# Performance work log

Hardware: AMD Instinct MI355X
Metric: run time of the kernel (lower is better)

The kernel has to match this reference:

```python
import jax, jax.numpy as jnp
import numpy as np

TEMPERATURE = 8.0

def _non_neg(x):
    # exp(x) for x<0, x+1 for x>=0 (non-negative feature map)
    return jnp.where(x < 0, jnp.exp(x), x + 1.0)

def setup_inputs() -> dict:
    key = jax.random.key(0)
    kq, kk, kv, km = jax.random.split(key, 4)
    B, H, S, D = 8, 16, 4096, 64
    q = jax.random.normal(kq, (B, H, S, D), dtype=jnp.float32)
    k = jax.random.normal(kk, (B, H, S, D), dtype=jnp.float32)
    v = jax.random.normal(kv, (B, H, S, D), dtype=jnp.float32)
    token_mask = jax.random.randint(km, (B, S), 0, 2).astype(bool)
    return {"q": q, "k": k, "v": v, "token_mask": token_mask}

def reference(q, k, v, token_mask):
    B, H, S, D = q.shape
    idx = jnp.arange(S, dtype=q.dtype)
    cos_vec = jnp.cos(jnp.pi / 2.0 / S * idx)[:, None]  # [S,1], broadcasts over D
    sin_vec = jnp.sin(jnp.pi / 2.0 / S * idx)[:, None]
    qf = _non_neg(q)
    kf = _non_neg(k)
    q_cos = qf * cos_vec
    q_sin = qf * sin_vec
    k_cos = kf * cos_vec
    k_sin = kf * sin_vec
    mask = token_mask[:, None, :, None].astype(q.dtype)  # [B,1,S,1]
    q_cos = q_cos * mask
    q_sin = q_sin * mask
    # global context: [B,H,D,Dv]
    k_cos_v = jnp.einsum('bhsd,bhse->bhde', k_cos, v)
    k_sin_v = jnp.einsum('bhsd,bhse->bhde', k_sin, v)
    values = (jnp.einsum('bhsd,bhde->bhse', q_cos, k_cos_v)
              + jnp.einsum('bhsd,bhde->bhse', q_sin, k_sin_v)) / TEMPERATURE
    return values
```

## Files before the change

kernel.cpp:

```cpp
#include <hip/hip_runtime.h>
#include <math.h>

#define Bn 8
#define Hn 16
#define Sn 4096
#define Dn 64
#define BHn 128
#define CW 3.834951969714103e-4f

typedef __attribute__((ext_vector_type(8))) short short8;
typedef __attribute__((ext_vector_type(4))) float f32x4;

__device__ __forceinline__ unsigned short f2bf(float x) {
    unsigned int u = __float_as_uint(x);
    u += 0x7fffu + ((u >> 16) & 1u);
    return (unsigned short)(u >> 16);
}
__device__ __forceinline__ unsigned int pack2(float lo, float hi) {
    return (unsigned int)f2bf(lo) | ((unsigned int)f2bf(hi) << 16);
}
__device__ __forceinline__ float nneg(float x) {
    return x < 0.f ? __expf(x) : x + 1.f;
}

__global__ __launch_bounds__(256) void k_init(float4* kv4, int* flag,
                                              const unsigned char* mask_raw) {
    int i = blockIdx.x * 256 + threadIdx.x;
    kv4[i] = make_float4(0.f, 0.f, 0.f, 0.f);
    if (blockIdx.x == 0) {
        __shared__ int s_any;
        if (threadIdx.x == 0) s_any = 0;
        __syncthreads();
        int any = 0;
        int base = threadIdx.x * 16;
        #pragma unroll
        for (int j = 0; j < 16; j++) {
            int idx = base + j;
            if ((idx & 3) && mask_raw[idx]) any = 1;
        }
        if (any) s_any = 1;
        __syncthreads();
        if (threadIdx.x == 0) *flag = s_any ? 0 : 1;
    }
}

__global__ __launch_bounds__(256) void k_phase1(const float* __restrict__ kk,
                                                const float* __restrict__ vv,
                                                float* __restrict__ kv) {
    __shared__ unsigned int ldsKc[64 * 36];
    __shared__ unsigned int ldsKs[64 * 36];
    __shared__ unsigned int ldsV [64 * 36];
    const int t    = threadIdx.x;
    const int bh   = blockIdx.x >> 3;
    const int sblk = (blockIdx.x & 7) << 9;
    const int c    = t & 15;
    const int rp   = t >> 4;
    const int lane = t & 63;
    const int w    = t >> 6;
    const int n    = lane & 15;
    const int q4   = lane >> 4;
    const float* kb = kk + (size_t)bh * (Sn * Dn);
    const float* vb = vv + (size_t)bh * (Sn * Dn);
    const unsigned short* ldsKc_h = (const unsigned short*)ldsKc;
    const unsigned short* ldsKs_h = (const unsigned short*)ldsKs;
    const unsigned short* ldsV_h  = (const unsigned short*)ldsV;

    f32x4 accC[4], accS[4];
    #pragma unroll
    for (int i = 0; i < 4; i++) {
        accC[i] = (f32x4){0.f, 0.f, 0.f, 0.f};
        accS[i] = (f32x4){0.f, 0.f, 0.f, 0.f};
    }

    for (int chunk = 0; chunk < 8; chunk++) {
        const int s0 = sblk + chunk * 64;
        #pragma unroll
        for (int half = 0; half < 2; half++) {
            int r0  = half * 32 + rp * 2;
            int s_a = s0 + r0, s_b = s0 + r0 + 1;
            float4 ka  = *(const float4*)(kb + (size_t)s_a * Dn + c * 4);
            float4 kb4 = *(const float4*)(kb + (size_t)s_b * Dn + c * 4);
            float4 va  = *(const float4*)(vb + (size_t)s_a * Dn + c * 4);
            float4 vb4 = *(const float4*)(vb + (size_t)s_b * Dn + c * 4);
            float csa, sna, csb, snb;
            __sincosf(CW * (float)s_a, &sna, &csa);
            __sincosf(CW * (float)s_b, &snb, &csb);
            float fa[4] = {nneg(ka.x),  nneg(ka.y),  nneg(ka.z),  nneg(ka.w)};
            float fb[4] = {nneg(kb4.x), nneg(kb4.y), nneg(kb4.z), nneg(kb4.w)};
            float ga[4] = {va.x, va.y, va.z, va.w};
            float gb[4] = {vb4.x, vb4.y, vb4.z, vb4.w};
            int sp = half * 16 + rp;
            #pragma unroll
            for (int j = 0; j < 4; j++) {
                int d = c * 4 + j;
                ldsKc[d * 36 + sp] = pack2(fa[j] * csa, fb[j] * csb);
                ldsKs[d * 36 + sp] = pack2(fa[j] * sna, fb[j] * snb);
                ldsV [d * 36 + sp] = pack2(ga[j],        gb[j]);
            }
        }
        __syncthreads();
        #pragma unroll
        for (int ks = 0; ks < 2; ks++) {
            short8 Bv = *(const short8*)(ldsV_h + (w * 16 + n) * 72 + ks * 32 + q4 * 8);
            #pragma unroll
            for (int dt = 0; dt < 4; dt++) {
                short8 Ac = *(const short8*)(ldsKc_h + (dt * 16 + n) * 72 + ks * 32 + q4 * 8);
                short8 As = *(const short8*)(ldsKs_h + (dt * 16 + n) * 72 + ks * 32 + q4 * 8);
                accC[dt] = __builtin_amdgcn_mfma_f32_16x16x32_bf16(Ac, Bv, accC[dt], 0, 0, 0);
                accS[dt] = __builtin_amdgcn_mfma_f32_16x16x32_bf16(As, Bv, accS[dt], 0, 0, 0);
            }
        }
        __syncthreads();
    }
    float* base = kv + (size_t)bh * 2 * 4096;
    int e = w * 16 + n;
    #pragma unroll
    for (int dt = 0; dt < 4; dt++) {
        #pragma unroll
        for (int r = 0; r < 4; r++) {
            int d = dt * 16 + q4 * 4 + r;
            atomicAdd(base +        e * 64 + d, accC[dt][r]);
            atomicAdd(base + 4096 + e * 64 + d, accS[dt][r]);
        }
    }
}

__global__ __launch_bounds__(256) void k_phase2(const float* __restrict__ qq,
                                                const void* __restrict__ mask_raw,
                                                const float* __restrict__ kv,
                                                const int* __restrict__ flag,
                                                float* __restrict__ out) {
    __shared__ unsigned int ldsC[64 * 36];
    __shared__ unsigned int ldsS[64 * 36];
    const int t    = threadIdx.x;
    const int bh   = blockIdx.x >> 3;
    const int sblk = (blockIdx.x & 7) << 9;
    const int b    = bh >> 4;
    const int lane = t & 63;
    const int w    = t >> 6;
    const int n    = lane & 15;
    const int q4   = lane >> 4;
    const int iflag = *flag;

    const float* kvb = kv + (size_t)bh * 2 * 4096;
    for (int i = t; i < 2048; i += 256) {
        int e = i >> 5, dp = i & 31;
        float2 xc = *(const float2*)(kvb +        e * 64 + dp * 2);
        float2 xs = *(const float2*)(kvb + 4096 + e * 64 + dp * 2);
        ldsC[e * 36 + dp] = pack2(xc.x, xc.y);
        ldsS[e * 36 + dp] = pack2(xs.x, xs.y);
    }
    __syncthreads();
    const unsigned short* ldsC_h = (const unsigned short*)ldsC;
    const unsigned short* ldsS_h = (const unsigned short*)ldsS;
    short8 Bc[4][2], Bs[4][2];
    #pragma unroll
    for (int et = 0; et < 4; et++) {
        #pragma unroll
        for (int ks = 0; ks < 2; ks++) {
            Bc[et][ks] = *(const short8*)(ldsC_h + (et * 16 + n) * 72 + ks * 32 + q4 * 8);
            Bs[et][ks] = *(const short8*)(ldsS_h + (et * 16 + n) * 72 + ks * 32 + q4 * 8);
        }
    }

    const float* qb = qq + (size_t)bh * (Sn * Dn);
    float* ob       = out + (size_t)bh * (Sn * Dn);
    const unsigned char* m8 = (const unsigned char*)mask_raw;
    const int* m32          = (const int*)mask_raw;

    for (int strip = 0; strip < 8; strip++) {
        int s_base = sblk + (strip * 4 + w) * 16;
        int s_row  = s_base + n;
        float mval;
        if (iflag) mval = m32[b * Sn + s_row] ? 1.f : 0.f;
        else       mval = m8 [b * Sn + s_row] ? 1.f : 0.f;
        float cs, sn;
        __sincosf(CW * (float)s_row, &sn, &cs);
        cs *= mval; sn *= mval;
        const float* qp = qb + (size_t)s_row * 64 + q4 * 8;
        float4 q0 = *(const float4*)(qp);
        float4 q1 = *(const float4*)(qp + 4);
        float4 q2 = *(const float4*)(qp + 32);
        float4 q3 = *(const float4*)(qp + 36);
        float f[16];
        f[0]=nneg(q0.x); f[1]=nneg(q0.y); f[2]=nneg(q0.z); f[3]=nneg(q0.w);
        f[4]=nneg(q1.x); f[5]=nneg(q1.y); f[6]=nneg(q1.z); f[7]=nneg(q1.w);
        f[8]=nneg(q2.x); f[9]=nneg(q2.y); f[10]=nneg(q2.z); f[11]=nneg(q2.w);
        f[12]=nneg(q3.x); f[13]=nneg(q3.y); f[14]=nneg(q3.z); f[15]=nneg(q3.w);
        short8 Ac0, As0, Ac1, As1;
        #pragma unroll
        for (int j = 0; j < 8; j++) {
            Ac0[j] = (short)f2bf(f[j] * cs);
            As0[j] = (short)f2bf(f[j] * sn);
            Ac1[j] = (short)f2bf(f[8 + j] * cs);
            As1[j] = (short)f2bf(f[8 + j] * sn);
        }
        f32x4 acc[4];
        #pragma unroll
        for (int et = 0; et < 4; et++) acc[et] = (f32x4){0.f, 0.f, 0.f, 0.f};
        #pragma unroll
        for (int et = 0; et < 4; et++) {
            acc[et] = __builtin_amdgcn_mfma_f32_16x16x32_bf16(Ac0, Bc[et][0], acc[et], 0, 0, 0);
            acc[et] = __builtin_amdgcn_mfma_f32_16x16x32_bf16(Ac1, Bc[et][1], acc[et], 0, 0, 0);
            acc[et] = __builtin_amdgcn_mfma_f32_16x16x32_bf16(As0, Bs[et][0], acc[et], 0, 0, 0);
            acc[et] = __builtin_amdgcn_mfma_f32_16x16x32_bf16(As1, Bs[et][1], acc[et], 0, 0, 0);
        }
        #pragma unroll
        for (int et = 0; et < 4; et++) {
            #pragma unroll
            for (int r = 0; r < 4; r++) {
                int row = q4 * 4 + r;
                ob[(size_t)(s_base + row) * 64 + et * 16 + n] = acc[et][r] * 0.125f;
            }
        }
    }
}

extern "C" void kernel_launch(void* const* d_in, const int* in_sizes, int n_in,
                              void* d_out, int out_size, void* d_ws, size_t ws_size,
                              hipStream_t stream) {
    const float* q = (const float*)d_in[0];
    const float* k = (const float*)d_in[1];
    const float* v = (const float*)d_in[2];
    const void* mask = d_in[3];
    int*   flag = (int*)d_ws;
    float* kv   = (float*)((char*)d_ws + 256);

    k_init  <<<1024, 256, 0, stream>>>((float4*)kv, flag, (const unsigned char*)mask);
    k_phase1<<<1024, 256, 0, stream>>>(k, v, kv);
    k_phase2<<<1024, 256, 0, stream>>>(q, mask, kv, flag, (float*)d_out);
}
```

Baseline: 506.0 us.

## Double-buffer global loads, double grid size, and transpose KV context layout

Both phases now launch twice as many blocks, each covering 256 sequence positions instead of 512. Loads for the next chunk or strip are issued into registers before the MFMA work on the current one, so global latency overlaps compute. Phase 1 writes wider packed LDS stores with a narrower row stride, and stores the context transposed (d-major). That lets phase 2 read its B fragments straight from global memory without an LDS staging pass and barrier. In exchange, phase 1 issues twice as many atomics, register pressure rises, and phase 2's per-element global gathers may be less coalesced.

```diff
diff --git a/kernel.cpp b/kernel.cpp
--- a/kernel.cpp
+++ b/kernel.cpp
@@ -1,12 +1,10 @@
 #include <hip/hip_runtime.h>
 #include <math.h>
 
-#define Bn 8
-#define Hn 16
 #define Sn 4096
 #define Dn 64
-#define BHn 128
 #define CW 3.834951969714103e-4f
+#define P1S 34
 
 typedef __attribute__((ext_vector_type(8))) short short8;
 typedef __attribute__((ext_vector_type(4))) float f32x4;
@@ -21,6 +19,13 @@
 }
 __device__ __forceinline__ float nneg(float x) {
     return x < 0.f ? __expf(x) : x + 1.f;
+}
+__device__ __forceinline__ short8 ld_frag(const unsigned int* p) {
+    uint2 a = *(const uint2*)p;
+    uint2 b = *(const uint2*)(p + 2);
+    union { unsigned int u[4]; short8 s; } r;
+    r.u[0] = a.x; r.u[1] = a.y; r.u[2] = b.x; r.u[3] = b.y;
+    return r.s;
 }
 
 __global__ __launch_bounds__(256) void k_init(float4* kv4, int* flag,
@@ -47,12 +52,12 @@
 __global__ __launch_bounds__(256) void k_phase1(const float* __restrict__ kk,
                                                 const float* __restrict__ vv,
                                                 float* __restrict__ kv) {
-    __shared__ unsigned int ldsKc[64 * 36];
-    __shared__ unsigned int ldsKs[64 * 36];
-    __shared__ unsigned int ldsV [64 * 36];
+    __shared__ unsigned int ldsKc[64 * P1S];
+    __shared__ unsigned int ldsKs[64 * P1S];
+    __shared__ unsigned int ldsV [64 * P1S];
     const int t    = threadIdx.x;
-    const int bh   = blockIdx.x >> 3;
-    const int sblk = (blockIdx.x & 7) << 9;
+    const int bh   = blockIdx.x >> 4;
+    const int sblk = (blockIdx.x & 15) << 8;
     const int c    = t & 15;
     const int rp   = t >> 4;
     const int lane = t & 63;
@@ -61,9 +66,6 @@
     const int q4   = lane >> 4;
     const float* kb = kk + (size_t)bh * (Sn * Dn);
     const float* vb = vv + (size_t)bh * (Sn * Dn);
-    const unsigned short* ldsKc_h = (const unsigned short*)ldsKc;
-    const unsigned short* ldsKs_h = (const unsigned short*)ldsKs;
-    const unsigned short* ldsV_h  = (const unsigned short*)ldsV;
 
     f32x4 accC[4], accS[4];
     #pragma unroll
@@ -72,40 +74,61 @@
         accS[i] = (f32x4){0.f, 0.f, 0.f, 0.f};
     }
 
-    for (int chunk = 0; chunk < 8; chunk++) {
+    float4 pk[2][4], pv[2][4];
+    {
+        const float* kp = kb + (size_t)(sblk + rp * 4) * Dn + c * 4;
+        const float* vp = vb + (size_t)(sblk + rp * 4) * Dn + c * 4;
+        #pragma unroll
+        for (int i = 0; i < 4; i++) {
+            pk[0][i] = *(const float4*)(kp + i * Dn);
+            pv[0][i] = *(const float4*)(vp + i * Dn);
+        }
+    }
+
+    #pragma unroll
+    for (int chunk = 0; chunk < 4; chunk++) {
+        const int cur = chunk & 1, nxt = cur ^ 1;
         const int s0 = sblk + chunk * 64;
-        #pragma unroll
-        for (int half = 0; half < 2; half++) {
-            int r0  = half * 32 + rp * 2;
-            int s_a = s0 + r0, s_b = s0 + r0 + 1;
-            float4 ka  = *(const float4*)(kb + (size_t)s_a * Dn + c * 4);
-            float4 kb4 = *(const float4*)(kb + (size_t)s_b * Dn + c * 4);
-            float4 va  = *(const float4*)(vb + (size_t)s_a * Dn + c * 4);
-            float4 vb4 = *(const float4*)(vb + (size_t)s_b * Dn + c * 4);
-            float csa, sna, csb, snb;
-            __sincosf(CW * (float)s_a, &sna, &csa);
-            __sincosf(CW * (float)s_b, &snb, &csb);
-            float fa[4] = {nneg(ka.x),  nneg(ka.y),  nneg(ka.z),  nneg(ka.w)};
-            float fb[4] = {nneg(kb4.x), nneg(kb4.y), nneg(kb4.z), nneg(kb4.w)};
-            float ga[4] = {va.x, va.y, va.z, va.w};
-            float gb[4] = {vb4.x, vb4.y, vb4.z, vb4.w};
-            int sp = half * 16 + rp;
-            #pragma unroll
-            for (int j = 0; j < 4; j++) {
-                int d = c * 4 + j;
-                ldsKc[d * 36 + sp] = pack2(fa[j] * csa, fb[j] * csb);
-                ldsKs[d * 36 + sp] = pack2(fa[j] * sna, fb[j] * snb);
-                ldsV [d * 36 + sp] = pack2(ga[j],        gb[j]);
-            }
-        }
-        __syncthreads();
+        float cs[4], sn[4], fk[4][4], fv[4][4];
+        #pragma unroll
+        for (int i = 0; i < 4; i++) {
+            __sincosf(CW * (float)(s0 + rp * 4 + i), &sn[i], &cs[i]);
+            fk[i][0] = nneg(pk[cur][i].x); fk[i][1] = nneg(pk[cur][i].y);
+            fk[i][2] = nneg(pk[cur][i].z); fk[i][3] = nneg(pk[cur][i].w);
+            fv[i][0] = pv[cur][i].x; fv[i][1] = pv[cur][i].y;
+            fv[i][2] = pv[cur][i].z; fv[i][3] = pv[cur][i].w;
+        }
+        #pragma unroll
+        for (int j = 0; j < 4; j++) {
+            int d = c * 4 + j;
+            uint2 wc, wsn, wv;
+            wc.x  = pack2(fk[0][j] * cs[0], fk[1][j] * cs[1]);
+            wc.y  = pack2(fk[2][j] * cs[2], fk[3][j] * cs[3]);
+            wsn.x = pack2(fk[0][j] * sn[0], fk[1][j] * sn[1]);
+            wsn.y = pack2(fk[2][j] * sn[2], fk[3][j] * sn[3]);
+            wv.x  = pack2(fv[0][j], fv[1][j]);
+            wv.y  = pack2(fv[2][j], fv[3][j]);
+            *(uint2*)&ldsKc[d * P1S + rp * 2] = wc;
+            *(uint2*)&ldsKs[d * P1S + rp * 2] = wsn;
+            *(uint2*)&ldsV [d * P1S + rp * 2] = wv;
+        }
+        __syncthreads();
+        if (chunk < 3) {
+            const float* kp = kb + (size_t)(s0 + 64 + rp * 4) * Dn + c * 4;
+            const float* vp = vb + (size_t)(s0 + 64 + rp * 4) * Dn + c * 4;
+            #pragma unroll
+            for (int i = 0; i < 4; i++) {
+                pk[nxt][i] = *(const float4*)(kp + i * Dn);
+                pv[nxt][i] = *(const float4*)(vp + i * Dn);
+            }
+        }
         #pragma unroll
         for (int ks = 0; ks < 2; ks++) {
-            short8 Bv = *(const short8*)(ldsV_h + (w * 16 + n) * 72 + ks * 32 + q4 * 8);
+            short8 Bv = ld_frag(&ldsV[(w * 16 + n) * P1S + ks * 16 + q4 * 4]);
             #pragma unroll
             for (int dt = 0; dt < 4; dt++) {
-                short8 Ac = *(const short8*)(ldsKc_h + (dt * 16 + n) * 72 + ks * 32 + q4 * 8);
-                short8 As = *(const short8*)(ldsKs_h + (dt * 16 + n) * 72 + ks * 32 + q4 * 8);
+                short8 Ac = ld_frag(&ldsKc[(dt * 16 + n) * P1S + ks * 16 + q4 * 4]);
+                short8 As = ld_frag(&ldsKs[(dt * 16 + n) * P1S + ks * 16 + q4 * 4]);
                 accC[dt] = __builtin_amdgcn_mfma_f32_16x16x32_bf16(Ac, Bv, accC[dt], 0, 0, 0);
                 accS[dt] = __builtin_amdgcn_mfma_f32_16x16x32_bf16(As, Bv, accS[dt], 0, 0, 0);
             }
@@ -113,14 +136,14 @@
         __syncthreads();
     }
     float* base = kv + (size_t)bh * 2 * 4096;
-    int e = w * 16 + n;
+    const int e = w * 16 + n;
     #pragma unroll
     for (int dt = 0; dt < 4; dt++) {
         #pragma unroll
         for (int r = 0; r < 4; r++) {
             int d = dt * 16 + q4 * 4 + r;
-            atomicAdd(base +        e * 64 + d, accC[dt][r]);
-            atomicAdd(base + 4096 + e * 64 + d, accS[dt][r]);
+            atomicAdd(base +        d * 64 + e, accC[dt][r]);
+            atomicAdd(base + 4096 + d * 64 + e, accS[dt][r]);
         }
     }
 }
@@ -130,11 +153,9 @@
                                                 const float* __restrict__ kv,
                                                 const int* __restrict__ flag,
                                                 float* __restrict__ out) {
-    __shared__ unsigned int ldsC[64 * 36];
-    __shared__ unsigned int ldsS[64 * 36];
     const int t    = threadIdx.x;
-    const int bh   = blockIdx.x >> 3;
-    const int sblk = (blockIdx.x & 7) << 9;
+    const int bh   = blockIdx.x >> 4;
+    const int sblk = (blockIdx.x & 15) << 8;
     const int b    = bh >> 4;
     const int lane = t & 63;
     const int w    = t >> 6;
@@ -142,24 +163,26 @@
     const int q4   = lane >> 4;
     const int iflag = *flag;
 
-    const float* kvb = kv + (size_t)bh * 2 * 4096;
-    for (int i = t; i < 2048; i += 256) {
-        int e = i >> 5, dp = i & 31;
-        float2 xc = *(const float2*)(kvb +        e * 64 + dp * 2);
-        float2 xs = *(const float2*)(kvb + 4096 + e * 64 + dp * 2);
-        ldsC[e * 36 + dp] = pack2(xc.x, xc.y);
-        ldsS[e * 36 + dp] = pack2(xs.x, xs.y);
-    }
-    __syncthreads();
-    const unsigned short* ldsC_h = (const unsigned short*)ldsC;
-    const unsigned short* ldsS_h = (const unsigned short*)ldsS;
+    const float* kvb = kv + (size_t)bh * 8192;
     short8 Bc[4][2], Bs[4][2];
     #pragma unroll
     for (int et = 0; et < 4; et++) {
+        const int e = et * 16 + n;
         #pragma unroll
         for (int ks = 0; ks < 2; ks++) {
-            Bc[et][ks] = *(const short8*)(ldsC_h + (et * 16 + n) * 72 + ks * 32 + q4 * 8);
-            Bs[et][ks] = *(const short8*)(ldsS_h + (et * 16 + n) * 72 + ks * 32 + q4 * 8);
+            const int d0 = ks * 32 + q4 * 8;
+            union { unsigned int u[4]; short8 s; } uc, us;
+            #pragma unroll
+            for (int jj = 0; jj < 4; jj++) {
+                float c0 = kvb[(size_t)(d0 + 2 * jj)     * 64 + e];
+                float c1 = kvb[(size_t)(d0 + 2 * jj + 1) * 64 + e];
+                float s0 = kvb[4096 + (size_t)(d0 + 2 * jj)     * 64 + e];
+                float s1 = kvb[4096 + (size_t)(d0 + 2 * jj + 1) * 64 + e];
+                uc.u[jj] = pack2(c0, c1);
+                us.u[jj] = pack2(s0, s1);
+            }
+            Bc[et][ks] = uc.s;
+            Bs[et][ks] = us.s;
         }
     }
 
@@ -168,32 +191,53 @@
     const unsigned char* m8 = (const unsigned char*)mask_raw;
     const int* m32          = (const int*)mask_raw;
 
-    for (int strip = 0; strip < 8; strip++) {
-        int s_base = sblk + (strip * 4 + w) * 16;
-        int s_row  = s_base + n;
-        float mval;
-        if (iflag) mval = m32[b * Sn + s_row] ? 1.f : 0.f;
-        else       mval = m8 [b * Sn + s_row] ? 1.f : 0.f;
-        float cs, sn;
-        __sincosf(CW * (float)s_row, &sn, &cs);
-        cs *= mval; sn *= mval;
-        const float* qp = qb + (size_t)s_row * 64 + q4 * 8;
-        float4 q0 = *(const float4*)(qp);
-        float4 q1 = *(const float4*)(qp + 4);
-        float4 q2 = *(const float4*)(qp + 32);
-        float4 q3 = *(const float4*)(qp + 36);
+    float4 pq[2][4];
+    float  pmv[2];
+    {
+        int s_row = sblk + w * 16 + n;
+        const float* qp = qb + (size_t)s_row * Dn + q4 * 8;
+        pq[0][0] = *(const float4*)(qp);
+        pq[0][1] = *(const float4*)(qp + 4);
+        pq[0][2] = *(const float4*)(qp + 32);
+        pq[0][3] = *(const float4*)(qp + 36);
+        pmv[0] = iflag ? (m32[b * Sn + s_row] ? 1.f : 0.f)
+                       : (m8 [b * Sn + s_row] ? 1.f : 0.f);
+    }
+
+    #pragma unroll
+    for (int strip = 0; strip < 4; strip++) {
+        const int cur = strip & 1, nxt = cur ^ 1;
+        const int s_base = sblk + strip * 64 + w * 16;
+        const int s_row  = s_base + n;
+        float cs, snv;
+        __sincosf(CW * (float)s_row, &snv, &cs);
+        cs *= pmv[cur]; snv *= pmv[cur];
         float f[16];
-        f[0]=nneg(q0.x); f[1]=nneg(q0.y); f[2]=nneg(q0.z); f[3]=nneg(q0.w);
-        f[4]=nneg(q1.x); f[5]=nneg(q1.y); f[6]=nneg(q1.z); f[7]=nneg(q1.w);
-        f[8]=nneg(q2.x); f[9]=nneg(q2.y); f[10]=nneg(q2.z); f[11]=nneg(q2.w);
-        f[12]=nneg(q3.x); f[13]=nneg(q3.y); f[14]=nneg(q3.z); f[15]=nneg(q3.w);
+        f[0]  = nneg(pq[cur][0].x); f[1]  = nneg(pq[cur][0].y);
+        f[2]  = nneg(pq[cur][0].z); f[3]  = nneg(pq[cur][0].w);
+        f[4]  = nneg(pq[cur][1].x); f[5]  = nneg(pq[cur][1].y);
+        f[6]  = nneg(pq[cur][1].z); f[7]  = nneg(pq[cur][1].w);
+        f[8]  = nneg(pq[cur][2].x); f[9]  = nneg(pq[cur][2].y);
+        f[10] = nneg(pq[cur][2].z); f[11] = nneg(pq[cur][2].w);
+        f[12] = nneg(pq[cur][3].x); f[13] = nneg(pq[cur][3].y);
+        f[14] = nneg(pq[cur][3].z); f[15] = nneg(pq[cur][3].w);
         short8 Ac0, As0, Ac1, As1;
         #pragma unroll
         for (int j = 0; j < 8; j++) {
             Ac0[j] = (short)f2bf(f[j] * cs);
-            As0[j] = (short)f2bf(f[j] * sn);
+            As0[j] = (short)f2bf(f[j] * snv);
             Ac1[j] = (short)f2bf(f[8 + j] * cs);
-            As1[j] = (short)f2bf(f[8 + j] * sn);
+            As1[j] = (short)f2bf(f[8 + j] * snv);
+        }
+        if (strip < 3) {
+            int s_row2 = sblk + (strip + 1) * 64 + w * 16 + n;
+            const float* qp = qb + (size_t)s_row2 * Dn + q4 * 8;
+            pq[nxt][0] = *(const float4*)(qp);
+            pq[nxt][1] = *(const float4*)(qp + 4);
+            pq[nxt][2] = *(const float4*)(qp + 32);
+            pq[nxt][3] = *(const float4*)(qp + 36);
+            pmv[nxt] = iflag ? (m32[b * Sn + s_row2] ? 1.f : 0.f)
+                             : (m8 [b * Sn + s_row2] ? 1.f : 0.f);
         }
         f32x4 acc[4];
         #pragma unroll
@@ -227,6 +271,6 @@
     float* kv   = (float*)((char*)d_ws + 256);
 
     k_init  <<<1024, 256, 0, stream>>>((float4*)kv, flag, (const unsigned char*)mask);
-    k_phase1<<<1024, 256, 0, stream>>>(k, v, kv);
-    k_phase2<<<1024, 256, 0, stream>>>(q, mask, kv, flag, (float*)d_out);
-}
+    k_phase1<<<2048, 256, 0, stream>>>(k, v, kv);
+    k_phase2<<<2048, 256, 0, stream>>>(q, mask, kv, flag, (float*)d_out);
+}
```

Measured after the change: 424.4 us. 1.19x faster.
